# Kernel tuning notes

Measured on AMD Instinct MI355X. Metric: run time of the kernel, lower is better.

## Reference

```python
import jax, jax.numpy as jnp
import numpy as np

B, LQ, LKV, D = 8, 2048, 2048, 1024

def setup_inputs() -> dict:
    key = jax.random.key(0)
    k1, k2, k3, k4, k5, k6, k7 = jax.random.split(key, 7)
    s = 1.0 / np.sqrt(D)
    return {
        "query": jax.random.normal(k1, (B, LQ, D), jnp.float32),
        "key": jax.random.normal(k2, (B, LKV, D), jnp.float32),
        "value": jax.random.normal(k3, (B, LKV, D), jnp.float32),
        "Wq": jax.random.uniform(k4, (D, D), jnp.float32, -s, s),
        "bq": jax.random.uniform(k5, (D,), jnp.float32, -s, s),
        "Wk": jax.random.uniform(k6, (D, D), jnp.float32, -s, s),
        "bk": jax.random.uniform(k7, (D,), jnp.float32, -s, s),
        "scale_factor": 32,
        "dropout_p": 0,
    }

def reference(query, key, value, Wq, bq, Wk, bk, scale_factor, dropout_p):
    # q/k linear projections (torch Linear: x @ W^T + b); v is used raw per the source
    q = jnp.einsum("bld,ed->ble", query, Wq) + bq
    k = jnp.einsum("bld,ed->ble", key, Wk) + bk
    scores = jnp.einsum("bqd,bkd->bqk", q, k) / jnp.float32(scale_factor)
    attn = jax.nn.softmax(scores, axis=-1)
    # dropout_p == 0 -> identity (deterministic baseline)
    return jnp.einsum("bqk,bkd->bqd", attn, value)
```

## Files before the change

kernel.cpp:

```cpp
#include <hip/hip_runtime.h>

typedef __bf16 bf16;
typedef __attribute__((ext_vector_type(4))) __bf16 bf16x4;
typedef __attribute__((ext_vector_type(8))) __bf16 bf16x8;
typedef __attribute__((ext_vector_type(4))) float f32x4;

__device__ __forceinline__ void gload_lds16(const void* g, void* l) {
  __builtin_amdgcn_global_load_lds(
      (const __attribute__((address_space(1))) unsigned int*)(unsigned long long)g,
      (__attribute__((address_space(3))) unsigned int*)(unsigned long long)l,
      16, 0, 0);
}

__global__ void cast_f32_bf16(const float* __restrict__ in, bf16* __restrict__ out, int n4) {
  int i = blockIdx.x * blockDim.x + threadIdx.x;
  if (i >= n4) return;
  float4 v = reinterpret_cast<const float4*>(in)[i];
  bf16x4 o;
  o[0] = (bf16)v.x; o[1] = (bf16)v.y; o[2] = (bf16)v.z; o[3] = (bf16)v.w;
  reinterpret_cast<bf16x4*>(out)[i] = o;
}

__global__ void transpose_cast(const float* __restrict__ V, bf16* __restrict__ VT,
                               int rows, int cols) {
  __shared__ bf16 tile[64][65];
  const int b = blockIdx.z;
  const float* Vb = V + (long)b * rows * cols;
  bf16* VTb = VT + (long)b * rows * cols;
  const int d0 = blockIdx.x * 64;
  const int k0 = blockIdx.y * 64;
  const int t = threadIdx.x;
  const int r = t >> 4;
  const int c4 = (t & 15) * 4;
#pragma unroll
  for (int p = 0; p < 4; ++p) {
    float4 v = *reinterpret_cast<const float4*>(&Vb[(long)(k0 + p * 16 + r) * cols + d0 + c4]);
    tile[p * 16 + r][c4 + 0] = (bf16)v.x;
    tile[p * 16 + r][c4 + 1] = (bf16)v.y;
    tile[p * 16 + r][c4 + 2] = (bf16)v.z;
    tile[p * 16 + r][c4 + 3] = (bf16)v.w;
  }
  __syncthreads();
#pragma unroll
  for (int p = 0; p < 4; ++p) {
    const int dd = p * 16 + r;
    bf16x4 o;
    o[0] = tile[c4 + 0][dd];
    o[1] = tile[c4 + 1][dd];
    o[2] = tile[c4 + 2][dd];
    o[3] = tile[c4 + 3][dd];
    *reinterpret_cast<bf16x4*>(&VTb[(long)(d0 + dd) * rows + k0 + c4]) = o;
  }
}

__global__ void softmax_rows(bf16* __restrict__ S) {
  const long row = blockIdx.x;
  bf16* p = S + row * 2048;
  const int t = threadIdx.x;
  const int wid = t >> 6;
  const int lane = t & 63;
  bf16x8 v = *reinterpret_cast<bf16x8*>(p + t * 8);
  float f[8];
  float m = -3.0e38f;
#pragma unroll
  for (int j = 0; j < 8; ++j) { f[j] = (float)v[j]; m = fmaxf(m, f[j]); }
#pragma unroll
  for (int off = 32; off >= 1; off >>= 1) m = fmaxf(m, __shfl_xor(m, off));
  __shared__ float redm[4], reds[4];
  if (lane == 0) redm[wid] = m;
  __syncthreads();
  m = fmaxf(fmaxf(redm[0], redm[1]), fmaxf(redm[2], redm[3]));
  float s = 0.f;
#pragma unroll
  for (int j = 0; j < 8; ++j) { f[j] = __expf(f[j] - m); s += f[j]; }
#pragma unroll
  for (int off = 32; off >= 1; off >>= 1) s += __shfl_xor(s, off);
  if (lane == 0) reds[wid] = s;
  __syncthreads();
  s = reds[0] + reds[1] + reds[2] + reds[3];
  const float inv = 1.0f / s;
  bf16x8 o;
#pragma unroll
  for (int j = 0; j < 8; ++j) o[j] = (bf16)(f[j] * inv);
  *reinterpret_cast<bf16x8*>(p + t * 8) = o;
}


#define BARRIER __builtin_amdgcn_s_barrier()
#define LGKM0                                              \
  do {                                                     \
    asm volatile("s_waitcnt lgkmcnt(0)" ::: "memory");     \
    __builtin_amdgcn_sched_barrier(0);                     \
  } while (0)
#define VM0                                                \
  do {                                                     \
    asm volatile("s_waitcnt vmcnt(0)" ::: "memory");       \
    __builtin_amdgcn_sched_barrier(0);                     \
  } while (0)

#define STAGE_A(buf, ko)                                        \
  {                                                             \
    bf16* l_ = ldsd + (buf) * 32768;                            \
    const bf16* g_ = gA + (ko);                                 \
    gload_lds16(g_, l_);                                        \
    gload_lds16(g_ + rK64, l_ + 4096);                          \
    gload_lds16(g_ + rK128, l_ + 8192);                         \
    gload_lds16(g_ + rK128 + rK64, l_ + 12288);                 \
  }
#define STAGE_B(buf, ko)                                        \
  {                                                             \
    bf16* l_ = ldsd + (buf) * 32768 + 16384;                    \
    const bf16* g_ = gB + (ko);                                 \
    gload_lds16(g_, l_);                                        \
    gload_lds16(g_ + rK64, l_ + 4096);                          \
    gload_lds16(g_ + rK128, l_ + 8192);                         \
    gload_lds16(g_ + rK128 + rK64, l_ + 12288);                 \
  }

#define LOADA(buf, mq)                                                        \
  {                                                                           \
    const bf16* p_ = aBase + (buf) * 32768 + (mq) * 4096;                     \
    _Pragma("unroll") for (int m_ = 0; m_ < 4; ++m_) {                        \
      a[m_][0] = *reinterpret_cast<const bf16x8*>(p_ + m_ * 1024 + pk0);      \
      a[m_][1] = *reinterpret_cast<const bf16x8*>(p_ + m_ * 1024 + pk1);      \
    }                                                                         \
  }
#define LOADB(buf, nq)                                                        \
  {                                                                           \
    const bf16* p_ = bBase + (buf) * 32768 + (nq) * 2048;                     \
    _Pragma("unroll") for (int n_ = 0; n_ < 2; ++n_) {                        \
      b[(nq) * 2 + n_][0] = *reinterpret_cast<const bf16x8*>(p_ + n_ * 1024 + pk0); \
      b[(nq) * 2 + n_][1] = *reinterpret_cast<const bf16x8*>(p_ + n_ * 1024 + pk1); \
    }                                                                         \
  }

#define MFMAQ(mq, nq)                                                         \
  _Pragma("unroll") for (int m_ = 0; m_ < 4; ++m_)                            \
  _Pragma("unroll") for (int n_ = 0; n_ < 2; ++n_)                            \
  _Pragma("unroll") for (int ks_ = 0; ks_ < 2; ++ks_)                         \
      acc[(mq) * 4 + m_][(nq) * 2 + n_] =                                     \
          __builtin_amdgcn_mfma_f32_16x16x32_bf16(                            \
              a[m_][ks_], b[(nq) * 2 + n_][ks_],                              \
              acc[(mq) * 4 + m_][(nq) * 2 + n_], 0, 0, 0);

template <int MODE>
__global__ __launch_bounds__(512, 2)
void gemm_bt(const bf16* __restrict__ A, const bf16* __restrict__ Bm,
             void* __restrict__ Cvoid, const int* __restrict__ scale_ptr,
             int N, int K, long sA, long sB, long sC) {
  __shared__ bf16 lds[2][2][2][128][64];
  const int t = threadIdx.x;
  const int lane = t & 63;
  const int wid = t >> 6;
  const int wm = wid >> 2;
  const int wn = wid & 3;

  const int gx = gridDim.x, gy = gridDim.y;
  const int nwg = gx * gy * gridDim.z;
  int id = blockIdx.x + gx * (blockIdx.y + gy * blockIdx.z);
  {
    const int cpx = nwg >> 3;
    id = (id & 7) * cpx + (id >> 3);
  }
  const int bx = id % gx;
  const int by = (id / gx) % gy;
  const int bz = id / (gx * gy);

  const bf16* Ab = A + (long)bz * sA;
  const bf16* Bb = Bm + (long)bz * sB;
  const int tile_m = by * 256;
  const int tile_n = bx * 256;

  const int srow = t >> 3;
  const int skc = t & 7;
  const int soff = ((skc ^ (srow & 7)) << 3);
  const bf16* gA = Ab + (long)(tile_m + srow) * K + soff;
  const bf16* gB = Bb + (long)(tile_n + srow) * K + soff;
  const long rK64 = (long)K << 6;
  const long rK128 = (long)K << 7;
  bf16* const ldsd = &lds[0][0][0][0][0] + wid * 512;

  const int frow = lane & 15;
  const int pk0 = (((lane >> 4) ^ (lane & 7))) << 3;
  const int pk1 = (((4 | (lane >> 4)) ^ (lane & 7))) << 3;
  const bf16* aBase = &lds[0][0][wm][frow][0];
  const bf16* bBase = &lds[0][1][wn >> 1][(wn & 1) * 64 + frow][0];

  bf16x8 a[4][2], b[4][2];
  f32x4 acc[8][4] = {};

  STAGE_A(0, 0)
  STAGE_B(0, 0)
  VM0;
  BARRIER;

  const int NK = K >> 6;
  int c = 0;
  for (int kt = 0; kt < NK - 1; ++kt, c ^= 1) {
    const long ko = (long)(kt + 1) << 6;
    LOADA(c, 0)
    LOADB(c, 0)
    STAGE_A(c ^ 1, ko)
    BARRIER;
    LGKM0;
    __builtin_amdgcn_s_setprio(1);
    MFMAQ(0, 0)
    __builtin_amdgcn_s_setprio(0);
    BARRIER;
    LOADB(c, 1)
    STAGE_B(c ^ 1, ko)
    BARRIER;
    LGKM0;
    __builtin_amdgcn_s_setprio(1);
    MFMAQ(0, 1)
    __builtin_amdgcn_s_setprio(0);
    BARRIER;
    LOADA(c, 1)
    BARRIER;
    LGKM0;
    __builtin_amdgcn_s_setprio(1);
    MFMAQ(1, 0)
    __builtin_amdgcn_s_setprio(0);
    BARRIER;
    VM0;
    BARRIER;
    __builtin_amdgcn_s_setprio(1);
    MFMAQ(1, 1)
    __builtin_amdgcn_s_setprio(0);
  }
  LOADA(c, 0)
  LOADB(c, 0)
  LOADB(c, 1)
  MFMAQ(0, 0)
  MFMAQ(0, 1)
  LOADA(c, 1)
  MFMAQ(1, 0)
  MFMAQ(1, 1)

  float scl = 1.0f;
  if (MODE == 1) {
    const int iv = scale_ptr[0];
    const float fv = __int_as_float(iv);
    const float sv = (iv > 0 && iv < (1 << 20)) ? (float)iv : fv;
    scl = 1.0f / sv;
  }
  const int rb = tile_m + wm * 128 + ((lane >> 4) << 2);
  const int cb = tile_n + wn * 64 + (lane & 15);
  if (MODE == 2) {
    float* C = reinterpret_cast<float*>(Cvoid) + (long)bz * sC;
#pragma unroll
    for (int mf = 0; mf < 8; ++mf)
#pragma unroll
      for (int nf = 0; nf < 4; ++nf)
#pragma unroll
        for (int r = 0; r < 4; ++r)
          C[(long)(rb + mf * 16 + r) * N + (cb + nf * 16)] = acc[mf][nf][r];
  } else {
    bf16* C = reinterpret_cast<bf16*>(Cvoid) + (long)bz * sC;
#pragma unroll
    for (int nf = 0; nf < 4; ++nf) {
      const int col = cb + nf * 16;
#pragma unroll
      for (int mf = 0; mf < 8; ++mf)
#pragma unroll
        for (int r = 0; r < 4; ++r)
          C[(long)(rb + mf * 16 + r) * N + col] = (bf16)(acc[mf][nf][r] * scl);
    }
  }
}

__global__ __launch_bounds__(512, 2)
void gemm_proj(const float* __restrict__ Aq, const float* __restrict__ Ak,
               const bf16* __restrict__ Wb, const float* __restrict__ bias0,
               const float* __restrict__ bias1, bf16* __restrict__ Cout,
               int N, int K, long sB, long sC) {
  __shared__ bf16 lds[2][12288];
  const int t = threadIdx.x;
  const int lane = t & 63;
  const int wid = t >> 6;
  const int wm = wid >> 2;
  const int wn = wid & 3;

  const int gx = gridDim.x, gy = gridDim.y;
  const int nwg = gx * gy * gridDim.z;
  int id = blockIdx.x + gx * (blockIdx.y + gy * blockIdx.z);
  {
    const int cpx = nwg >> 3;
    id = (id & 7) * cpx + (id >> 3);
  }
  const int bx = id % gx;
  const int by = (id / gx) % gy;
  const int bz = id / (gx * gy);

  const float* Af = bz ? Ak : Aq;
  const bf16* Bb = Wb + (long)bz * sB;
  const int tile_m = by * 128;
  const int tile_n = bx * 256;

  const int arow = t >> 2;
  const int akc = t & 3;
  const float* gAf = Af + (long)(tile_m + arow) * K + akc * 8;
  bf16* const wA = &lds[0][0] + arow * 32 + (((akc ^ ((t >> 3) & 3))) << 3);

  const int srow = t >> 2;
  const int soff = (((t & 3) ^ ((t >> 3) & 3)) << 3);
  const bf16* gB = Bb + (long)(tile_n + srow) * K + soff;
  const long rK128 = (long)K << 7;
  bf16* const ldsB = &lds[0][4096] + wid * 512;

  const int frow = lane & 15;
  const int pko = (((lane >> 4) ^ ((lane >> 1) & 3)) << 3);
  const bf16* aB = &lds[0][0] + (wm * 64 + frow) * 32 + pko;
  const bf16* bB = &lds[0][4096] + (wn * 64 + frow) * 32 + pko;

  bf16x8 a[4], b[4];
  f32x4 acc[4][4] = {};

  {
    float4 p0 = *reinterpret_cast<const float4*>(gAf);
    float4 p1 = *reinterpret_cast<const float4*>(gAf + 4);
    gload_lds16(gB, ldsB);
    gload_lds16(gB + rK128, ldsB + 4096);
    bf16x8 w;
    w[0] = (bf16)p0.x; w[1] = (bf16)p0.y; w[2] = (bf16)p0.z; w[3] = (bf16)p0.w;
    w[4] = (bf16)p1.x; w[5] = (bf16)p1.y; w[6] = (bf16)p1.z; w[7] = (bf16)p1.w;
    *reinterpret_cast<bf16x8*>(wA) = w;
    __syncthreads();
  }

  const int NK = K >> 5;
  int c = 0;
  for (int kt = 0; kt < NK - 1; ++kt, c ^= 1) {
    const long ko = (long)(kt + 1) << 5;
    float4 n0 = *reinterpret_cast<const float4*>(gAf + ko);
    float4 n1 = *reinterpret_cast<const float4*>(gAf + ko + 4);
    gload_lds16(gB + ko, ldsB + (c ^ 1) * 12288);
    gload_lds16(gB + ko + rK128, ldsB + (c ^ 1) * 12288 + 4096);
#pragma unroll
    for (int n_ = 0; n_ < 4; ++n_)
      b[n_] = *reinterpret_cast<const bf16x8*>(bB + c * 12288 + n_ * 512);
#pragma unroll
    for (int m_ = 0; m_ < 4; ++m_)
      a[m_] = *reinterpret_cast<const bf16x8*>(aB + c * 12288 + m_ * 512);
#pragma unroll
    for (int m_ = 0; m_ < 4; ++m_)
#pragma unroll
      for (int n_ = 0; n_ < 4; ++n_)
        acc[m_][n_] = __builtin_amdgcn_mfma_f32_16x16x32_bf16(a[m_], b[n_], acc[m_][n_], 0, 0, 0);
    {
      bf16x8 w;
      w[0] = (bf16)n0.x; w[1] = (bf16)n0.y; w[2] = (bf16)n0.z; w[3] = (bf16)n0.w;
      w[4] = (bf16)n1.x; w[5] = (bf16)n1.y; w[6] = (bf16)n1.z; w[7] = (bf16)n1.w;
      *reinterpret_cast<bf16x8*>(wA + (c ^ 1) * 12288) = w;
    }
    __syncthreads();
  }
#pragma unroll
  for (int n_ = 0; n_ < 4; ++n_)
    b[n_] = *reinterpret_cast<const bf16x8*>(bB + c * 12288 + n_ * 512);
#pragma unroll
  for (int m_ = 0; m_ < 4; ++m_)
    a[m_] = *reinterpret_cast<const bf16x8*>(aB + c * 12288 + m_ * 512);
#pragma unroll
  for (int m_ = 0; m_ < 4; ++m_)
#pragma unroll
    for (int n_ = 0; n_ < 4; ++n_)
      acc[m_][n_] = __builtin_amdgcn_mfma_f32_16x16x32_bf16(a[m_], b[n_], acc[m_][n_], 0, 0, 0);

  const float* bias = bz ? bias1 : bias0;
  const int rb = tile_m + wm * 64 + ((lane >> 4) << 2);
  const int cb = tile_n + wn * 64 + (lane & 15);
  bf16* C = Cout + (long)bz * sC;
#pragma unroll
  for (int nf = 0; nf < 4; ++nf) {
    const int col = cb + nf * 16;
    const float bv = bias[col];
#pragma unroll
    for (int mf = 0; mf < 4; ++mf)
#pragma unroll
      for (int r = 0; r < 4; ++r)
        C[(long)(rb + mf * 16 + r) * N + col] = (bf16)(acc[mf][nf][r] + bv);
  }
}

extern "C" void kernel_launch(void* const* d_in, const int* in_sizes, int n_in,
                              void* d_out, int out_size, void* d_ws, size_t ws_size,
                              hipStream_t stream) {
  (void)in_sizes; (void)n_in; (void)out_size; (void)ws_size;
  const float* query = (const float*)d_in[0];
  const float* key   = (const float*)d_in[1];
  const float* value = (const float*)d_in[2];
  const float* Wq    = (const float*)d_in[3];
  const float* bq    = (const float*)d_in[4];
  const float* Wk    = (const float*)d_in[5];
  const float* bk    = (const float*)d_in[6];
  const int*   scale = (const int*)d_in[7];

  const int L = 2048, D = 1024;
  char* ws = (char*)d_ws;
  bf16* S      = (bf16*)ws;
  bf16* Qp     = (bf16*)(ws + (size_t)67108864);
  bf16* Kp     = (bf16*)(ws + (size_t)100663296);
  bf16* VT     = (bf16*)(ws + (size_t)134217728);
  bf16* Wqb    = (bf16*)(ws + (size_t)167772160);
  bf16* Wkb    = (bf16*)(ws + (size_t)169869312);

  cast_f32_bf16<<<1024, 256, 0, stream>>>(Wq, Wqb, 262144);
  cast_f32_bf16<<<1024, 256, 0, stream>>>(Wk, Wkb, 262144);
  transpose_cast<<<dim3(16, 32, 8), 256, 0, stream>>>(value, VT, 2048, 1024);

  gemm_proj<<<dim3(4, 128, 2), 512, 0, stream>>>(query, key, Wqb, bq, bk, Qp,
                                                 1024, 1024, 1048576L, 16777216L);
  gemm_bt<1><<<dim3(8, 8, 8), 512, 0, stream>>>(Qp, Kp, S, scale,
                                                2048, 1024,
                                                (long)L * D, (long)L * D, (long)L * L);
  softmax_rows<<<16384, 256, 0, stream>>>(S);
  gemm_bt<2><<<dim3(4, 8, 8), 512, 0, stream>>>(S, VT, d_out, nullptr,
                                                1024, 2048,
                                                (long)L * L, (long)D * L, (long)L * D);
}
```

Before: 296.8 us.

## Stream fp32 A tiles directly to LDS and convert at fragment load

The projection GEMM now copies the fp32 activation tile straight into LDS with global_load_lds, using an XOR swizzle. It converts to bf16 when each wave reads its MFMA fragments, replacing the register-staged load, convert and LDS store. This frees registers and shortens the prefetch path. The cost is that LDS per block grows to 64KB and every wave repeats the conversion for the A data it shares with other waves. The launch bounds hint also rises to 4 blocks per CU, which LDS capacity cannot satisfy and which may force tight register limits and spilling.

```diff
diff --git a/kernel.cpp b/kernel.cpp
--- a/kernel.cpp
+++ b/kernel.cpp
@@ -269,12 +269,12 @@
   }
 }
 
-__global__ __launch_bounds__(512, 2)
+__global__ __launch_bounds__(512, 4)
 void gemm_proj(const float* __restrict__ Aq, const float* __restrict__ Ak,
                const bf16* __restrict__ Wb, const float* __restrict__ bias0,
                const float* __restrict__ bias1, bf16* __restrict__ Cout,
                int N, int K, long sB, long sC) {
-  __shared__ bf16 lds[2][12288];
+  __shared__ bf16 lds[32768];
   const int t = threadIdx.x;
   const int lane = t & 63;
   const int wid = t >> 6;
@@ -297,70 +297,80 @@
   const int tile_m = by * 128;
   const int tile_n = bx * 256;
 
-  const int arow = t >> 2;
-  const int akc = t & 3;
-  const float* gAf = Af + (long)(tile_m + arow) * K + akc * 8;
-  bf16* const wA = &lds[0][0] + arow * 32 + (((akc ^ ((t >> 3) & 3))) << 3);
-
-  const int srow = t >> 2;
-  const int soff = (((t & 3) ^ ((t >> 3) & 3)) << 3);
-  const bf16* gB = Bb + (long)(tile_n + srow) * K + soff;
+  const int ar = t >> 3;
+  const int akc = t & 7;
+  const float* gA0 = Af + (long)(tile_m + ar) * K + ((akc ^ (ar & 7)) << 2);
+  const long aK64 = (long)K << 6;
+  float* const ldsAf = reinterpret_cast<float*>(&lds[0]);
+  float* const aDst = ldsAf + wid * 256;
+
+  const int br = t >> 2;
+  const int bkc = t & 3;
+  const bf16* gB0 = Bb + (long)(tile_n + br) * K + ((bkc ^ ((br >> 1) & 3)) << 3);
   const long rK128 = (long)K << 7;
-  bf16* const ldsB = &lds[0][4096] + wid * 512;
+  bf16* const bDst = &lds[8192 * 2] + wid * 512;
+
 
   const int frow = lane & 15;
-  const int pko = (((lane >> 4) ^ ((lane >> 1) & 3)) << 3);
-  const bf16* aB = &lds[0][0] + (wm * 64 + frow) * 32 + pko;
-  const bf16* bB = &lds[0][4096] + (wn * 64 + frow) * 32 + pko;
+  const int fj = lane >> 4;
+  const int pa0 = (((2 * fj) ^ (frow & 7)) << 2);
+  const int pa1 = (((2 * fj + 1) ^ (frow & 7)) << 2);
+  const float* aF = ldsAf + (wm * 64 + frow) * 32;
+  const int pko = ((fj ^ ((lane >> 1) & 3)) << 3);
+  const bf16* bF = &lds[8192] + (wn * 64 + frow) * 32 + pko;
+  bf16* const bDstFix = &lds[8192] + wid * 512;
 
   bf16x8 a[4], b[4];
   f32x4 acc[4][4] = {};
 
-  {
-    float4 p0 = *reinterpret_cast<const float4*>(gAf);
-    float4 p1 = *reinterpret_cast<const float4*>(gAf + 4);
-    gload_lds16(gB, ldsB);
-    gload_lds16(gB + rK128, ldsB + 4096);
-    bf16x8 w;
-    w[0] = (bf16)p0.x; w[1] = (bf16)p0.y; w[2] = (bf16)p0.z; w[3] = (bf16)p0.w;
-    w[4] = (bf16)p1.x; w[5] = (bf16)p1.y; w[6] = (bf16)p1.z; w[7] = (bf16)p1.w;
-    *reinterpret_cast<bf16x8*>(wA) = w;
-    __syncthreads();
-  }
+#define PSTAGE(buf, ko)                                                \
+  {                                                                    \
+    gload_lds16(gA0 + (ko), aDst + (buf) * 8192);                      \
+    gload_lds16(gA0 + (ko) + aK64, aDst + (buf) * 8192 + 2048);        \
+    gload_lds16(gB0 + (ko), bDstFix + (buf) * 16384);                  \
+    gload_lds16(gB0 + (ko) + rK128, bDstFix + (buf) * 16384 + 4096);   \
+  }
+
+  PSTAGE(0, 0)
+  __syncthreads();
 
   const int NK = K >> 5;
   int c = 0;
   for (int kt = 0; kt < NK - 1; ++kt, c ^= 1) {
-    const long ko = (long)(kt + 1) << 5;
-    float4 n0 = *reinterpret_cast<const float4*>(gAf + ko);
-    float4 n1 = *reinterpret_cast<const float4*>(gAf + ko + 4);
-    gload_lds16(gB + ko, ldsB + (c ^ 1) * 12288);
-    gload_lds16(gB + ko + rK128, ldsB + (c ^ 1) * 12288 + 4096);
+    PSTAGE(c ^ 1, (kt + 1) * 32)
 #pragma unroll
     for (int n_ = 0; n_ < 4; ++n_)
-      b[n_] = *reinterpret_cast<const bf16x8*>(bB + c * 12288 + n_ * 512);
-#pragma unroll
-    for (int m_ = 0; m_ < 4; ++m_)
-      a[m_] = *reinterpret_cast<const bf16x8*>(aB + c * 12288 + m_ * 512);
+      b[n_] = *reinterpret_cast<const bf16x8*>(bF + c * 16384 + n_ * 512);
+#pragma unroll
+    for (int m_ = 0; m_ < 4; ++m_) {
+      const float* p_ = aF + c * 8192 + m_ * 512;
+      float4 fa = *reinterpret_cast<const float4*>(p_ + pa0);
+      float4 fb = *reinterpret_cast<const float4*>(p_ + pa1);
+      bf16x8 av;
+      av[0] = (bf16)fa.x; av[1] = (bf16)fa.y; av[2] = (bf16)fa.z; av[3] = (bf16)fa.w;
+      av[4] = (bf16)fb.x; av[5] = (bf16)fb.y; av[6] = (bf16)fb.z; av[7] = (bf16)fb.w;
+      a[m_] = av;
+    }
 #pragma unroll
     for (int m_ = 0; m_ < 4; ++m_)
 #pragma unroll
       for (int n_ = 0; n_ < 4; ++n_)
         acc[m_][n_] = __builtin_amdgcn_mfma_f32_16x16x32_bf16(a[m_], b[n_], acc[m_][n_], 0, 0, 0);
-    {
-      bf16x8 w;
-      w[0] = (bf16)n0.x; w[1] = (bf16)n0.y; w[2] = (bf16)n0.z; w[3] = (bf16)n0.w;
-      w[4] = (bf16)n1.x; w[5] = (bf16)n1.y; w[6] = (bf16)n1.z; w[7] = (bf16)n1.w;
-      *reinterpret_cast<bf16x8*>(wA + (c ^ 1) * 12288) = w;
-    }
     __syncthreads();
   }
 #pragma unroll
   for (int n_ = 0; n_ < 4; ++n_)
-    b[n_] = *reinterpret_cast<const bf16x8*>(bB + c * 12288 + n_ * 512);
-#pragma unroll
-  for (int m_ = 0; m_ < 4; ++m_)
-    a[m_] = *reinterpret_cast<const bf16x8*>(aB + c * 12288 + m_ * 512);
+    b[n_] = *reinterpret_cast<const bf16x8*>(bF + c * 16384 + n_ * 512);
+#pragma unroll
+  for (int m_ = 0; m_ < 4; ++m_) {
+    const float* p_ = aF + c * 8192 + m_ * 512;
+    float4 fa = *reinterpret_cast<const float4*>(p_ + pa0);
+    float4 fb = *reinterpret_cast<const float4*>(p_ + pa1);
+    bf16x8 av;
+    av[0] = (bf16)fa.x; av[1] = (bf16)fa.y; av[2] = (bf16)fa.z; av[3] = (bf16)fa.w;
+    av[4] = (bf16)fb.x; av[5] = (bf16)fb.y; av[6] = (bf16)fb.z; av[7] = (bf16)fb.w;
+    a[m_] = av;
+  }
 #pragma unroll
   for (int m_ = 0; m_ < 4; ++m_)
 #pragma unroll
@@ -381,6 +391,7 @@
       for (int r = 0; r < 4; ++r)
         C[(long)(rb + mf * 16 + r) * N + col] = (bf16)(acc[mf][nf][r] + bv);
   }
+#undef PSTAGE
 }
 
 extern "C" void kernel_launch(void* const* d_in, const int* in_sizes, int n_in,
```

Result: slower. 305.5 us (+2.9%).
